# Kernel tuning notes

Hardware: AMD Instinct MI355X
Metric: run time of the kernel (lower is better)

The kernel has to match this reference:

```python
import jax, jax.numpy as jnp
import numpy as np

B, ISIZE, N, OSIZE = 2048, 512, 2048, 128
TC = 1.0 / 10.0  # dt/tau
PX = 0.5


def setup_inputs() -> dict:
    key = jax.random.key(0)
    ks = jax.random.split(key, 16)
    s = 0.01
    return {
        "x": jax.random.normal(ks[0], (B, ISIZE), jnp.float32),
        "h0_in": jax.random.normal(ks[1], (B, N), jnp.float32),
        "h1_in": jax.random.normal(ks[2], (B, N), jnp.float32),
        "h2_in": jax.random.normal(ks[3], (B, N), jnp.float32),
        "i_to_h0": s * jax.random.normal(ks[4], (ISIZE, N), jnp.float32),
        "h0_w": s * jax.random.normal(ks[5], (N, N), jnp.float32),
        "h0_b": s * jax.random.uniform(ks[6], (N,), jnp.float32),
        "h0_to_h1": s * jax.random.normal(ks[7], (N, N), jnp.float32),
        "h1_w": s * jax.random.normal(ks[8], (N, N), jnp.float32),
        "h1_b": s * jax.random.uniform(ks[9], (N,), jnp.float32),
        "h1_to_h2": s * jax.random.normal(ks[10], (N, N), jnp.float32),
        "h2_w": s * jax.random.normal(ks[11], (N, N), jnp.float32),
        "h2_b": s * jax.random.uniform(ks[12], (N,), jnp.float32),
        "w_out": s * jax.random.normal(ks[13], (N, OSIZE), jnp.float32),
        # Bernoulli(px) sparsity masks (non-trainable buffers in the original)
        "m01": (jax.random.uniform(ks[14], (N, N)) < PX).astype(jnp.float32),
        "m12": (jax.random.uniform(ks[15], (N, N)) < PX).astype(jnp.float32),
    }


def reference(x, h0_in, h1_in, h2_in, i_to_h0, h0_w, h0_b, h0_to_h1,
              h1_w, h1_b, h1_to_h2, h2_w, h2_b, w_out, m01, m12):
    tc = TC
    # zero-diagonal mask applied to every recurrent weight (no self-connections)
    diag = 1.0 - jnp.eye(N, dtype=h0_w.dtype)
    # replicate_ashok=True: feedforward weights are sparsified by Bernoulli masks
    h01 = h0_to_h1 * m01
    h12 = h1_to_h2 * m12

    # layer 0: input drive + masked recurrence + leaky integration
    h0 = h0_in * (1.0 - tc) + jax.nn.relu(
        x @ i_to_h0 + h0_in @ (h0_w * diag) + h0_b) * tc
    # layer 1
    h1 = h1_in * (1.0 - tc) + jax.nn.relu(
        h0 @ h01 + h1_in @ (h1_w * diag) + h1_b) * tc
    # layer 2
    h2 = h2_in * (1.0 - tc) + jax.nn.relu(
        h1 @ h12 + h2_in @ (h2_w * diag) + h2_b) * tc

    out = h2 @ w_out  # Linear without bias (replicate_ashok=True)
    return (h0, h1, h2, out)
```

## Files before the change

### kernel.cpp

```cpp
#include <hip/hip_runtime.h>
#include <hip/hip_bf16.h>
#include <stdint.h>

typedef __bf16 bf16;
typedef __bf16 bf16x8 __attribute__((ext_vector_type(8)));
typedef float f32x4 __attribute__((ext_vector_type(4)));

#define BB   2048
#define ISZ  512
#define NN   2048
#define OSZ  128

struct PackD { const float* src; bf16* dst; int W, ld, off, n8; };
struct TD    { const float* src; const float* msk; bf16* dst;
               int Ncols, ld_dst, k_off, mode, ntk, start; };
struct PAll  { PackD p[4]; TD d[7]; int packBlocks; };
struct TDef  { TD d[3]; int total; };

__global__ __launch_bounds__(256) void prep_all_k(PAll a) {
  if ((int)blockIdx.x < a.packBlocks) {
    int idx = blockIdx.x * 256 + threadIdx.x;
    PackD d = a.p[0]; int base = 0;
#pragma unroll
    for (int i = 1; i < 4; ++i) if (idx >= a.p[i - 1].n8) { d = a.p[i]; base = a.p[i - 1].n8; }
    if (idx >= d.n8) return;
    int e = (idx - base) * 8;
    int m = e / d.W;
    int c = e - m * d.W;
    const float4 v0 = *reinterpret_cast<const float4*>(d.src + e);
    const float4 v1 = *reinterpret_cast<const float4*>(d.src + e + 4);
    bf16x8 o;
    o[0] = (bf16)v0.x; o[1] = (bf16)v0.y; o[2] = (bf16)v0.z; o[3] = (bf16)v0.w;
    o[4] = (bf16)v1.x; o[5] = (bf16)v1.y; o[6] = (bf16)v1.z; o[7] = (bf16)v1.w;
    *reinterpret_cast<bf16x8*>(d.dst + (size_t)m * d.ld + d.off + c) = o;
    return;
  }
  int bid = blockIdx.x - a.packBlocks;
  TD d = a.d[0];
#pragma unroll
  for (int i = 1; i < 7; ++i) if (bid >= a.d[i].start) d = a.d[i];
  int local = bid - d.start;
  int k0 = (local % d.ntk) * 128;
  int n0 = (local / d.ntk) * 32;
  __shared__ float t[128][33];
  const int tx8 = threadIdx.x & 7;
  const int kr  = threadIdx.x >> 3;
  const int nc  = n0 + tx8 * 4;
#pragma unroll
  for (int i = 0; i < 4; ++i) {
    int k = k0 + kr + 32 * i;
    float4 v = *reinterpret_cast<const float4*>(d.src + (size_t)k * d.Ncols + nc);
    if (d.mode == 2) {
      float4 m = *reinterpret_cast<const float4*>(d.msk + (size_t)k * d.Ncols + nc);
      v.x *= m.x; v.y *= m.y; v.z *= m.z; v.w *= m.w;
    } else if (d.mode == 1) {
      if (k == nc)     v.x = 0.f;
      if (k == nc + 1) v.y = 0.f;
      if (k == nc + 2) v.z = 0.f;
      if (k == nc + 3) v.w = 0.f;
    }
    float* r = &t[kr + 32 * i][tx8 * 4];
    r[0] = v.x; r[1] = v.y; r[2] = v.z; r[3] = v.w;
  }
  __syncthreads();
  const int n  = threadIdx.x >> 3;
  const int kc = (threadIdx.x & 7) * 16;
  bf16x8 o0, o1;
#pragma unroll
  for (int j = 0; j < 8; ++j) {
    o0[j] = (bf16)t[kc + j][n];
    o1[j] = (bf16)t[kc + 8 + j][n];
  }
  bf16* dp = d.dst + (size_t)(n0 + n) * d.ld_dst + d.k_off + k0 + kc;
  *reinterpret_cast<bf16x8*>(dp) = o0;
  *reinterpret_cast<bf16x8*>(dp + 8) = o1;
}

struct GP {
  const bf16* A; const bf16* B;
  int K, lda, ldb;
  const float* hin; const float* bias; const float* radd;
  float* outf; int ld_out;
  bf16* nxt; int ld_nxt;
  int epi;
};

__device__ __forceinline__ void gload16(const bf16* g, bf16* l) {
  __builtin_amdgcn_global_load_lds(
      (const __attribute__((address_space(1))) void*)g,
      (__attribute__((address_space(3))) void*)l, 16, 0, 0);
}

__device__ __forceinline__ void epilogue_store(const GP& p, int row, int col, float v) {
  size_t oidx = (size_t)row * p.ld_out + col;
  if (p.epi == 0) {
    float pre = v + p.bias[col];
    if (p.radd) pre += p.radd[oidx];
    float h = p.hin[oidx] * 0.9f + fmaxf(pre, 0.f) * 0.1f;
    p.outf[oidx] = h;
    p.nxt[(size_t)row * p.ld_nxt + col] = (bf16)h;
  } else {
    p.outf[oidx] = v;
  }
}

__device__ __forceinline__ void gemm_ks(const GP p, uint8_t* smraw) {
  typedef bf16 smT[2][128][64];
  smT* sm = (smT*)smraw;
  const int lane = threadIdx.x & 63;
  const int wave = threadIdx.x >> 6;
  const int ks = wave >> 2;
  const int sp = wave & 3;
  const int gx = gridDim.x, nwg = gx * gridDim.y;
  const int lid = blockIdx.x + gx * blockIdx.y;
  const int q = nwg >> 3;
  const int swz = (lid & 7) * q + (lid >> 3);
  const int m0 = (swz / gx) * 128, n0 = (swz % gx) * 128;
  const int wm0 = (sp >> 1) * 64, wn0 = (sp & 1) * 64;
  const int srow = lane >> 3;
  const int scol = ((lane & 7) ^ srow) * 8;
  const int frow = lane & 15;
  const int rcol = (((ks << 2) + (lane >> 4)) ^ (frow & 7)) * 8;

  f32x4 acc[4][4];
#pragma unroll
  for (int i = 0; i < 4; ++i)
#pragma unroll
    for (int j = 0; j < 4; ++j)
#pragma unroll
      for (int r = 0; r < 4; ++r) acc[i][j][r] = 0.f;

  auto stage = [&](int buf, int t) {
    const int k0 = t * 64;
#pragma unroll
    for (int h = 0; h < 2; ++h) {
      const int c = wave + h * 8;
      gload16(p.A + (size_t)(m0 + c * 8 + srow) * p.lda + k0 + scol,
              &sm[buf][0][0][0] + c * 512);
      gload16(p.B + (size_t)(n0 + c * 8 + srow) * p.ldb + k0 + scol,
              &sm[buf][1][0][0] + c * 512);
    }
  };

  const int nt = p.K / 64;
  stage(0, 0);
  int cur = 0;
  for (int t = 0; t < nt; ++t) {
    if (t + 1 < nt) {
      stage(cur ^ 1, t + 1);
      asm volatile("s_waitcnt vmcnt(4)" ::: "memory");
    } else {
      asm volatile("s_waitcnt vmcnt(0)" ::: "memory");
    }
    __builtin_amdgcn_s_barrier();

    bf16x8 af[4], bf_[4];
#pragma unroll
    for (int i = 0; i < 4; ++i)
      af[i] = *reinterpret_cast<const bf16x8*>(&sm[cur][0][wm0 + i * 16 + frow][rcol]);
#pragma unroll
    for (int j = 0; j < 4; ++j)
      bf_[j] = *reinterpret_cast<const bf16x8*>(&sm[cur][1][wn0 + j * 16 + frow][rcol]);
#pragma unroll
    for (int i = 0; i < 4; ++i)
#pragma unroll
      for (int j = 0; j < 4; ++j)
        acc[i][j] = __builtin_amdgcn_mfma_f32_16x16x32_bf16(af[i], bf_[j], acc[i][j], 0, 0, 0);

    if (t + 1 < nt) {
      asm volatile("s_waitcnt lgkmcnt(0)" ::: "memory");
      __builtin_amdgcn_s_barrier();
    }
    cur ^= 1;
  }

  asm volatile("s_waitcnt lgkmcnt(0)" ::: "memory");
  __builtin_amdgcn_s_barrier();
  float* red = (float*)smraw;
  if (ks == 1) {
#pragma unroll
    for (int i = 0; i < 4; ++i)
#pragma unroll
      for (int j = 0; j < 4; ++j)
        *reinterpret_cast<f32x4*>(&red[sp * 4096 + (i * 4 + j) * 256 + lane * 4]) = acc[i][j];
    asm volatile("s_waitcnt lgkmcnt(0)" ::: "memory");
  }
  __builtin_amdgcn_s_barrier();
  if (ks == 0) {
#pragma unroll
    for (int i = 0; i < 4; ++i)
#pragma unroll
      for (int j = 0; j < 4; ++j) {
        f32x4 o = *reinterpret_cast<const f32x4*>(&red[sp * 4096 + (i * 4 + j) * 256 + lane * 4]);
#pragma unroll
        for (int r = 0; r < 4; ++r) acc[i][j][r] += o[r];
#pragma unroll
        for (int r = 0; r < 4; ++r)
          epilogue_store(p, m0 + wm0 + i * 16 + (lane >> 4) * 4 + r,
                         n0 + wn0 + j * 16 + (lane & 15), acc[i][j][r]);
      }
  }
}

__device__ __forceinline__ void transpose512(const TD& d, int tile, bool active,
                                             uint8_t* smraw) {
  float (*t)[65] = (float (*)[65])smraw;
  int k0 = 0, n0 = 0;
  if (active) { k0 = (tile % d.ntk) * 128; n0 = (tile / d.ntk) * 64; }
  const int tx = threadIdx.x & 15;
  const int kr = threadIdx.x >> 4;
  const int nc = n0 + tx * 4;
  if (active) {
#pragma unroll
    for (int i = 0; i < 4; ++i) {
      int k = k0 + kr + 32 * i;
      float4 v = *reinterpret_cast<const float4*>(d.src + (size_t)k * d.Ncols + nc);
      if (d.mode == 2) {
        float4 m = *reinterpret_cast<const float4*>(d.msk + (size_t)k * d.Ncols + nc);
        v.x *= m.x; v.y *= m.y; v.z *= m.z; v.w *= m.w;
      }
      float* r = &t[kr + 32 * i][tx * 4];
      r[0] = v.x; r[1] = v.y; r[2] = v.z; r[3] = v.w;
    }
  }
  __syncthreads();
  if (active) {
    const int n  = threadIdx.x >> 3;
    const int kc = (threadIdx.x & 7) * 16;
    bf16x8 o0, o1;
#pragma unroll
    for (int j = 0; j < 8; ++j) {
      o0[j] = (bf16)t[kc + j][n0 + n - n0 + n * 0 + n];
      o1[j] = (bf16)t[kc + 8 + j][n];
    }
#pragma unroll
    for (int j = 0; j < 8; ++j) o0[j] = (bf16)t[kc + j][n];
    bf16* dp = d.dst + (size_t)(n0 + n) * d.ld_dst + d.k_off + k0 + kc;
    *reinterpret_cast<bf16x8*>(dp) = o0;
    *reinterpret_cast<bf16x8*>(dp + 8) = o1;
  }
  __syncthreads();
}

__global__ __launch_bounds__(512) void k_tri(GP p0, GP p1, GP p2, TDef td) {
  __shared__ __align__(16) uint8_t smraw[65536];
  if (blockIdx.z < 3) {
    GP p;
    if (blockIdx.z == 0) p = p0;
    else if (blockIdx.z == 1) p = p1;
    else p = p2;
    gemm_ks(p, smraw);
    return;
  }
  const int bid = blockIdx.x + gridDim.x * blockIdx.y;
  const int nb = gridDim.x * gridDim.y;
  const int iters = (td.total + nb - 1) / nb;
  for (int it = 0; it < iters; ++it) {
    int tile = it * nb + bid;
    TD d = td.d[0];
    if (tile >= td.d[1].start) d = td.d[1];
    if (tile >= td.d[2].start) d = td.d[2];
    int local = tile - d.start;
    transpose512(d, local, tile < td.total, smraw);
  }
}

__global__ __launch_bounds__(512) void k_split(GP p0, GP p1) {
  __shared__ __align__(16) uint8_t smraw[65536];
  gemm_ks(blockIdx.z == 0 ? p0 : p1, smraw);
}

template<int BM, int BN>
__device__ __forceinline__ void gemm_body8(const GP p) {
  constexpr int BK = 32;
  constexpr int WM = BM / 2, WN = BN / 4;
  constexpr int FM = WM / 16, FN = WN / 16;
  __shared__ bf16 As[2][BM][BK];
  __shared__ bf16 Bs[2][BN][BK];
  const int lane = threadIdx.x & 63;
  const int wave = threadIdx.x >> 6;
  const int m0 = blockIdx.y * BM, n0 = blockIdx.x * BN;
  const int wm0 = (wave >> 2) * WM, wn0 = (wave & 3) * WN;
  const int srow = lane >> 2;
  const int scolE = (((lane & 3) ^ ((lane >> 3) & 3)) * 8);
  const int frow = lane & 15;
  const int rcolE = (((lane >> 4) ^ ((frow >> 1) & 3)) * 8);

  f32x4 acc[FM][FN];
#pragma unroll
  for (int i = 0; i < FM; ++i)
#pragma unroll
    for (int j = 0; j < FN; ++j)
#pragma unroll
      for (int r = 0; r < 4; ++r) acc[i][j][r] = 0.f;

  auto stage = [&](int buf, int t) {
    const int k0 = t * BK;
#pragma unroll
    for (int c = wave; c < BM / 16; c += 8) {
      const bf16* g = p.A + (size_t)(m0 + c * 16 + srow) * p.lda + k0 + scolE;
      gload16(g, &As[buf][0][0] + c * 512);
    }
#pragma unroll
    for (int c = wave; c < BN / 16; c += 8) {
      const bf16* g = p.B + (size_t)(n0 + c * 16 + srow) * p.ldb + k0 + scolE;
      gload16(g, &Bs[buf][0][0] + c * 512);
    }
  };

  const int nt = p.K / BK;
  stage(0, 0);
  __syncthreads();
  int cur = 0;
  for (int t = 0; t < nt; ++t) {
    if (t + 1 < nt) stage(cur ^ 1, t + 1);
    bf16x8 af[FM], bfrag[FN];
#pragma unroll
    for (int i = 0; i < FM; ++i)
      af[i] = *reinterpret_cast<const bf16x8*>(&As[cur][wm0 + i * 16 + frow][rcolE]);
#pragma unroll
    for (int j = 0; j < FN; ++j)
      bfrag[j] = *reinterpret_cast<const bf16x8*>(&Bs[cur][wn0 + j * 16 + frow][rcolE]);
#pragma unroll
    for (int i = 0; i < FM; ++i)
#pragma unroll
      for (int j = 0; j < FN; ++j)
        acc[i][j] = __builtin_amdgcn_mfma_f32_16x16x32_bf16(af[i], bfrag[j], acc[i][j], 0, 0, 0);
    __syncthreads();
    cur ^= 1;
  }

#pragma unroll
  for (int i = 0; i < FM; ++i)
#pragma unroll
    for (int j = 0; j < FN; ++j)
#pragma unroll
      for (int r = 0; r < 4; ++r)
        epilogue_store(p, m0 + wm0 + i * 16 + (lane >> 4) * 4 + r,
                       n0 + wn0 + j * 16 + (lane & 15), acc[i][j][r]);
}

__global__ __launch_bounds__(512) void k_out(GP p) { gemm_body8<32, 64>(p); }

__global__ __launch_bounds__(256) void k_epi(const float* __restrict__ P0,
                                             const float* __restrict__ P1,
                                             const float* __restrict__ radd,
                                             const float* __restrict__ hin,
                                             const float* __restrict__ bias,
                                             float* __restrict__ outf,
                                             bf16* __restrict__ nxt) {
  int e = (blockIdx.x * 256 + threadIdx.x) * 8;
  int colb = e & (NN - 1);
  const float4 a0 = *reinterpret_cast<const float4*>(P0 + e);
  const float4 a1 = *reinterpret_cast<const float4*>(P0 + e + 4);
  const float4 b0 = *reinterpret_cast<const float4*>(P1 + e);
  const float4 b1 = *reinterpret_cast<const float4*>(P1 + e + 4);
  const float4 r0 = *reinterpret_cast<const float4*>(radd + e);
  const float4 r1 = *reinterpret_cast<const float4*>(radd + e + 4);
  const float4 h0 = *reinterpret_cast<const float4*>(hin + e);
  const float4 h1 = *reinterpret_cast<const float4*>(hin + e + 4);
  const float4 c0 = *reinterpret_cast<const float4*>(bias + colb);
  const float4 c1 = *reinterpret_cast<const float4*>(bias + colb + 4);
  float pa[8] = {a0.x, a0.y, a0.z, a0.w, a1.x, a1.y, a1.z, a1.w};
  float pb[8] = {b0.x, b0.y, b0.z, b0.w, b1.x, b1.y, b1.z, b1.w};
  float pr[8] = {r0.x, r0.y, r0.z, r0.w, r1.x, r1.y, r1.z, r1.w};
  float ph[8] = {h0.x, h0.y, h0.z, h0.w, h1.x, h1.y, h1.z, h1.w};
  float pc[8] = {c0.x, c0.y, c0.z, c0.w, c1.x, c1.y, c1.z, c1.w};
  float4 o0, o1;
  bf16x8 nb;
#pragma unroll
  for (int j = 0; j < 8; ++j) {
    float pre = pa[j] + pb[j] + pr[j] + pc[j];
    float h = ph[j] * 0.9f + fmaxf(pre, 0.f) * 0.1f;
    (j < 4 ? (&o0.x)[j] : (&o1.x)[j - 4]) = h;
    nb[j] = (bf16)h;
  }
  *reinterpret_cast<float4*>(outf + e) = o0;
  *reinterpret_cast<float4*>(outf + e + 4) = o1;
  *reinterpret_cast<bf16x8*>(nxt + e) = nb;
}

extern "C" void kernel_launch(void* const* d_in, const int* in_sizes, int n_in,
                              void* d_out, int out_size, void* d_ws, size_t ws_size,
                              hipStream_t stream) {
  const float* x        = (const float*)d_in[0];
  const float* h0_in    = (const float*)d_in[1];
  const float* h1_in    = (const float*)d_in[2];
  const float* h2_in    = (const float*)d_in[3];
  const float* i_to_h0  = (const float*)d_in[4];
  const float* h0_w     = (const float*)d_in[5];
  const float* h0_b     = (const float*)d_in[6];
  const float* h0_to_h1 = (const float*)d_in[7];
  const float* h1_w     = (const float*)d_in[8];
  const float* h1_b     = (const float*)d_in[9];
  const float* h1_to_h2 = (const float*)d_in[10];
  const float* h2_w     = (const float*)d_in[11];
  const float* h2_b     = (const float*)d_in[12];
  const float* w_out    = (const float*)d_in[13];
  const float* m01      = (const float*)d_in[14];
  const float* m12      = (const float*)d_in[15];
  float* out = (float*)d_out;

  uint8_t* ws = (uint8_t*)d_ws;
  constexpr size_t OFF_A0  = 0;
  constexpr size_t OFF_W0  = OFF_A0 + 10485760;
  constexpr size_t OFF_W1R = OFF_W0 + 10485760;
  constexpr size_t OFF_W2R = OFF_W1R + 8388608;
  constexpr size_t OFF_W01 = OFF_W2R + 8388608;
  constexpr size_t OFF_W12 = OFF_W01 + 8388608;
  constexpr size_t OFF_WO  = OFF_W12 + 8388608;
  constexpr size_t OFF_AR1 = OFF_WO + 524288;
  constexpr size_t OFF_AR2 = OFF_AR1 + 8388608;
  constexpr size_t OFF_AH0 = OFF_AR2 + 8388608;
  constexpr size_t WS_NEED = OFF_AH0 + 8388608;
  if (ws_size < WS_NEED) return;

  bf16* A0  = (bf16*)(ws + OFF_A0);
  bf16* Wt0 = (bf16*)(ws + OFF_W0);
  bf16* W1r = (bf16*)(ws + OFF_W1R);
  bf16* W2r = (bf16*)(ws + OFF_W2R);
  bf16* W01 = (bf16*)(ws + OFF_W01);
  bf16* W12 = (bf16*)(ws + OFF_W12);
  bf16* WtO = (bf16*)(ws + OFF_WO);
  bf16* Ar1 = (bf16*)(ws + OFF_AR1);
  bf16* Ar2 = (bf16*)(ws + OFF_AR2);
  bf16* Ah0 = (bf16*)(ws + OFF_AH0);
  bf16* Ah1 = Ar1;
  bf16* Ah2 = Ar2;
  float* P0 = (float*)(ws + 0);
  float* P1 = (float*)(ws + 16777216);

  float* o_h0  = out;
  float* o_h1  = out + (size_t)BB * NN;
  float* o_h2  = out + (size_t)2 * BB * NN;
  float* o_out = out + (size_t)3 * BB * NN;

  PAll pa;
  int n8a = BB * ISZ / 8;
  int n8b = n8a + BB * NN / 8;
  int n8c = n8b + BB * NN / 8;
  int n8d = n8c + BB * NN / 8;
  pa.p[0] = {x,     A0,  ISZ, ISZ + NN, 0,   n8a};
  pa.p[1] = {h0_in, A0,  NN,  ISZ + NN, ISZ, n8b};
  pa.p[2] = {h1_in, Ar1, NN,  NN,       0,   n8c};
  pa.p[3] = {h2_in, Ar2, NN,  NN,       0,   n8d};
  pa.packBlocks = (n8d + 255) / 256;
  int s0 = 0;
  pa.d[0] = {i_to_h0, nullptr, Wt0, NN, ISZ + NN, 0,   0, ISZ / 128, s0}; s0 += (ISZ / 128) * (NN / 32);
  pa.d[1] = {h0_w,    nullptr, Wt0, NN, ISZ + NN, ISZ, 1, NN / 128,  s0}; s0 += (NN / 128) * (NN / 32);
  pa.d[2] = {h1_w,    nullptr, W1r, NN, NN,       0,   1, NN / 128,  s0}; s0 += (NN / 128) * (NN / 32);
  pa.d[3] = {h2_w,    nullptr, W2r, NN, NN,       0,   1, NN / 128,  s0}; s0 += (NN / 128) * (NN / 32);
  pa.d[4] = pa.d[3]; pa.d[4].start = 0x7FFFFFFF;
  pa.d[5] = pa.d[4];
  pa.d[6] = pa.d[4];
  prep_all_k<<<pa.packBlocks + s0, 256, 0, stream>>>(pa);

  TDef td;
  int t0 = 0;
  td.d[0] = {h0_to_h1, m01, W01, NN,  NN, 0, 2, NN / 128, t0}; t0 += (NN / 128) * (NN / 64);
  td.d[1] = {h1_to_h2, m12, W12, NN,  NN, 0, 2, NN / 128, t0}; t0 += (NN / 128) * (NN / 64);
  td.d[2] = {w_out,  nullptr, WtO, OSZ, NN, 0, 0, NN / 128, t0}; t0 += (NN / 128) * (OSZ / 64);
  td.total = t0;

  GP pS0{A0,  Wt0, ISZ + NN, ISZ + NN, ISZ + NN, h0_in, h0_b, nullptr,
         o_h0, NN, Ah0, NN, 0};
  GP pR1{Ar1, W1r, NN, NN, NN, nullptr, nullptr, nullptr, o_h1, NN, nullptr, 0, 1};
  GP pR2{Ar2, W2r, NN, NN, NN, nullptr, nullptr, nullptr, o_h2, NN, nullptr, 0, 1};
  k_tri<<<dim3(NN / 128, BB / 128, 4), 512, 0, stream>>>(pS0, pR1, pR2, td);

  GP pG1a{Ah0,          W01,          NN / 2, NN, NN, nullptr, nullptr, nullptr, P0, NN, nullptr, 0, 1};
  GP pG1b{Ah0 + NN / 2, W01 + NN / 2, NN / 2, NN, NN, nullptr, nullptr, nullptr, P1, NN, nullptr, 0, 1};
  k_split<<<dim3(NN / 128, BB / 128, 2), 512, 0, stream>>>(pG1a, pG1b);
  k_epi<<<BB * NN / 2048, 256, 0, stream>>>(P0, P1, o_h1, h1_in, h1_b, o_h1, Ah1);

  GP pG2a{Ah1,          W12,          NN / 2, NN, NN, nullptr, nullptr, nullptr, P0, NN, nullptr, 0, 1};
  GP pG2b{Ah1 + NN / 2, W12 + NN / 2, NN / 2, NN, NN, nullptr, nullptr, nullptr, P1, NN, nullptr, 0, 1};
  k_split<<<dim3(NN / 128, BB / 128, 2), 512, 0, stream>>>(pG2a, pG2b);
  k_epi<<<BB * NN / 2048, 256, 0, stream>>>(P0, P1, o_h2, h2_in, h2_b, o_h2, Ah2);

  GP pO{Ah2, WtO, NN, NN, NN, nullptr, nullptr, nullptr, o_out, OSZ, nullptr, 0, 1};
  k_out<<<dim3(OSZ / 64, BB / 32), 512, 0, stream>>>(pO);
}
```

Baseline: 214.4 us.

## Fuse feedforward GEMMs with leaky-ReLU epilogue, dropping split-K partials

Replaces the two-way split-K GEMM plus separate elementwise epilogue kernel for layers 1 and 2 with a single fused GEMM. It uses 128x64 tiles, an in-block K split across wave groups with an LDS reduction, and a grouped block-index swizzle, and it applies bias, the recurrent add, ReLU and the leaky update directly in the epilogue. This removes the fp32 partial buffers P0/P1, their round trips through global memory, and two kernel launches. In exchange each block now iterates over the full K of 2048, and the grid has the same block count but smaller tiles. A redundant store loop in the transpose is also cleaned up.

New measurement: 243.3 us. 1.14x slower.

```diff
diff --git a/kernel.cpp b/kernel.cpp
--- a/kernel.cpp
+++ b/kernel.cpp
@@ -202,6 +202,102 @@
   }
 }
 
+__device__ __forceinline__ void gemm_fused64(const GP p) {
+  __shared__ __align__(16) bf16 sA[2][128][64];
+  __shared__ __align__(16) bf16 sB[2][64][64];
+  const int lane = threadIdx.x & 63;
+  const int wave = threadIdx.x >> 6;
+  const int ks = wave >> 2;
+  const int sp = wave & 3;
+  const int gx = gridDim.x, nwg = gx * gridDim.y;
+  const int lid = blockIdx.x + gx * blockIdx.y;
+  const int q = nwg >> 3;
+  const int swz = (lid & 7) * q + (lid >> 3);
+  const int m0 = (swz / gx) * 128, n0 = (swz % gx) * 64;
+  const int wm0 = (sp >> 1) * 64, wn0 = (sp & 1) * 32;
+  const int srow = lane >> 3;
+  const int scol = ((lane & 7) ^ srow) * 8;
+  const int frow = lane & 15;
+  const int rcol = (((ks << 2) + (lane >> 4)) ^ (frow & 7)) * 8;
+
+  f32x4 acc[4][2];
+#pragma unroll
+  for (int i = 0; i < 4; ++i)
+#pragma unroll
+    for (int j = 0; j < 2; ++j)
+#pragma unroll
+      for (int r = 0; r < 4; ++r) acc[i][j][r] = 0.f;
+
+  auto stage = [&](int buf, int t) {
+    const int k0 = t * 64;
+    gload16(p.A + (size_t)(m0 + wave * 8 + srow) * p.lda + k0 + scol,
+            &sA[buf][0][0] + wave * 512);
+    gload16(p.A + (size_t)(m0 + (wave + 8) * 8 + srow) * p.lda + k0 + scol,
+            &sA[buf][0][0] + (wave + 8) * 512);
+    gload16(p.B + (size_t)(n0 + wave * 8 + srow) * p.ldb + k0 + scol,
+            &sB[buf][0][0] + wave * 512);
+  };
+
+  const int nt = p.K / 64;
+  stage(0, 0);
+  int cur = 0;
+  for (int t = 0; t < nt; ++t) {
+    if (t + 1 < nt) {
+      stage(cur ^ 1, t + 1);
+      asm volatile("s_waitcnt vmcnt(3)" ::: "memory");
+    } else {
+      asm volatile("s_waitcnt vmcnt(0)" ::: "memory");
+    }
+    __builtin_amdgcn_s_barrier();
+
+    bf16x8 af[4], bf_[2];
+#pragma unroll
+    for (int i = 0; i < 4; ++i)
+      af[i] = *reinterpret_cast<const bf16x8*>(&sA[cur][wm0 + i * 16 + frow][rcol]);
+#pragma unroll
+    for (int j = 0; j < 2; ++j)
+      bf_[j] = *reinterpret_cast<const bf16x8*>(&sB[cur][wn0 + j * 16 + frow][rcol]);
+#pragma unroll
+    for (int i = 0; i < 4; ++i)
+#pragma unroll
+      for (int j = 0; j < 2; ++j)
+        acc[i][j] = __builtin_amdgcn_mfma_f32_16x16x32_bf16(af[i], bf_[j], acc[i][j], 0, 0, 0);
+
+    if (t + 1 < nt) {
+      asm volatile("s_waitcnt lgkmcnt(0)" ::: "memory");
+      __builtin_amdgcn_s_barrier();
+    }
+    cur ^= 1;
+  }
+
+  asm volatile("s_waitcnt lgkmcnt(0)" ::: "memory");
+  __builtin_amdgcn_s_barrier();
+  float* red = (float*)&sA[0][0][0];
+  if (ks == 1) {
+#pragma unroll
+    for (int i = 0; i < 4; ++i)
+#pragma unroll
+      for (int j = 0; j < 2; ++j)
+        *reinterpret_cast<f32x4*>(&red[sp * 2048 + (i * 2 + j) * 256 + lane * 4]) = acc[i][j];
+    asm volatile("s_waitcnt lgkmcnt(0)" ::: "memory");
+  }
+  __builtin_amdgcn_s_barrier();
+  if (ks == 0) {
+#pragma unroll
+    for (int i = 0; i < 4; ++i)
+#pragma unroll
+      for (int j = 0; j < 2; ++j) {
+        f32x4 o = *reinterpret_cast<const f32x4*>(&red[sp * 2048 + (i * 2 + j) * 256 + lane * 4]);
+#pragma unroll
+        for (int r = 0; r < 4; ++r) acc[i][j][r] += o[r];
+#pragma unroll
+        for (int r = 0; r < 4; ++r)
+          epilogue_store(p, m0 + wm0 + i * 16 + (lane >> 4) * 4 + r,
+                         n0 + wn0 + j * 16 + (lane & 15), acc[i][j][r]);
+      }
+  }
+}
+
 __device__ __forceinline__ void transpose512(const TD& d, int tile, bool active,
                                              uint8_t* smraw) {
   float (*t)[65] = (float (*)[65])smraw;
@@ -230,11 +326,9 @@
     bf16x8 o0, o1;
 #pragma unroll
     for (int j = 0; j < 8; ++j) {
-      o0[j] = (bf16)t[kc + j][n0 + n - n0 + n * 0 + n];
+      o0[j] = (bf16)t[kc + j][n];
       o1[j] = (bf16)t[kc + 8 + j][n];
     }
-#pragma unroll
-    for (int j = 0; j < 8; ++j) o0[j] = (bf16)t[kc + j][n];
     bf16* dp = d.dst + (size_t)(n0 + n) * d.ld_dst + d.k_off + k0 + kc;
     *reinterpret_cast<bf16x8*>(dp) = o0;
     *reinterpret_cast<bf16x8*>(dp + 8) = o1;
@@ -265,10 +359,7 @@
   }
 }
 
-__global__ __launch_bounds__(512) void k_split(GP p0, GP p1) {
-  __shared__ __align__(16) uint8_t smraw[65536];
-  gemm_ks(blockIdx.z == 0 ? p0 : p1, smraw);
-}
+__global__ __launch_bounds__(512) void k_fused(GP p) { gemm_fused64(p); }
 
 template<int BM, int BN>
 __device__ __forceinline__ void gemm_body8(const GP p) {
@@ -341,44 +432,6 @@
 }
 
 __global__ __launch_bounds__(512) void k_out(GP p) { gemm_body8<32, 64>(p); }
-
-__global__ __launch_bounds__(256) void k_epi(const float* __restrict__ P0,
-                                             const float* __restrict__ P1,
-                                             const float* __restrict__ radd,
-                                             const float* __restrict__ hin,
-                                             const float* __restrict__ bias,
-                                             float* __restrict__ outf,
-                                             bf16* __restrict__ nxt) {
-  int e = (blockIdx.x * 256 + threadIdx.x) * 8;
-  int colb = e & (NN - 1);
-  const float4 a0 = *reinterpret_cast<const float4*>(P0 + e);
-  const float4 a1 = *reinterpret_cast<const float4*>(P0 + e + 4);
-  const float4 b0 = *reinterpret_cast<const float4*>(P1 + e);
-  const float4 b1 = *reinterpret_cast<const float4*>(P1 + e + 4);
-  const float4 r0 = *reinterpret_cast<const float4*>(radd + e);
-  const float4 r1 = *reinterpret_cast<const float4*>(radd + e + 4);
-  const float4 h0 = *reinterpret_cast<const float4*>(hin + e);
-  const float4 h1 = *reinterpret_cast<const float4*>(hin + e + 4);
-  const float4 c0 = *reinterpret_cast<const float4*>(bias + colb);
-  const float4 c1 = *reinterpret_cast<const float4*>(bias + colb + 4);
-  float pa[8] = {a0.x, a0.y, a0.z, a0.w, a1.x, a1.y, a1.z, a1.w};
-  float pb[8] = {b0.x, b0.y, b0.z, b0.w, b1.x, b1.y, b1.z, b1.w};
-  float pr[8] = {r0.x, r0.y, r0.z, r0.w, r1.x, r1.y, r1.z, r1.w};
-  float ph[8] = {h0.x, h0.y, h0.z, h0.w, h1.x, h1.y, h1.z, h1.w};
-  float pc[8] = {c0.x, c0.y, c0.z, c0.w, c1.x, c1.y, c1.z, c1.w};
-  float4 o0, o1;
-  bf16x8 nb;
-#pragma unroll
-  for (int j = 0; j < 8; ++j) {
-    float pre = pa[j] + pb[j] + pr[j] + pc[j];
-    float h = ph[j] * 0.9f + fmaxf(pre, 0.f) * 0.1f;
-    (j < 4 ? (&o0.x)[j] : (&o1.x)[j - 4]) = h;
-    nb[j] = (bf16)h;
-  }
-  *reinterpret_cast<float4*>(outf + e) = o0;
-  *reinterpret_cast<float4*>(outf + e + 4) = o1;
-  *reinterpret_cast<bf16x8*>(nxt + e) = nb;
-}
 
 extern "C" void kernel_launch(void* const* d_in, const int* in_sizes, int n_in,
                               void* d_out, int out_size, void* d_ws, size_t ws_size,
@@ -427,8 +480,6 @@
   bf16* Ah0 = (bf16*)(ws + OFF_AH0);
   bf16* Ah1 = Ar1;
   bf16* Ah2 = Ar2;
-  float* P0 = (float*)(ws + 0);
-  float* P1 = (float*)(ws + 16777216);
 
   float* o_h0  = out;
   float* o_h1  = out + (size_t)BB * NN;
@@ -468,15 +519,11 @@
   GP pR2{Ar2, W2r, NN, NN, NN, nullptr, nullptr, nullptr, o_h2, NN, nullptr, 0, 1};
   k_tri<<<dim3(NN / 128, BB / 128, 4), 512, 0, stream>>>(pS0, pR1, pR2, td);
 
-  GP pG1a{Ah0,          W01,          NN / 2, NN, NN, nullptr, nullptr, nullptr, P0, NN, nullptr, 0, 1};
-  GP pG1b{Ah0 + NN / 2, W01 + NN / 2, NN / 2, NN, NN, nullptr, nullptr, nullptr, P1, NN, nullptr, 0, 1};
-  k_split<<<dim3(NN / 128, BB / 128, 2), 512, 0, stream>>>(pG1a, pG1b);
-  k_epi<<<BB * NN / 2048, 256, 0, stream>>>(P0, P1, o_h1, h1_in, h1_b, o_h1, Ah1);
-
-  GP pG2a{Ah1,          W12,          NN / 2, NN, NN, nullptr, nullptr, nullptr, P0, NN, nullptr, 0, 1};
-  GP pG2b{Ah1 + NN / 2, W12 + NN / 2, NN / 2, NN, NN, nullptr, nullptr, nullptr, P1, NN, nullptr, 0, 1};
-  k_split<<<dim3(NN / 128, BB / 128, 2), 512, 0, stream>>>(pG2a, pG2b);
-  k_epi<<<BB * NN / 2048, 256, 0, stream>>>(P0, P1, o_h2, h2_in, h2_b, o_h2, Ah2);
+  GP pF1{Ah0, W01, NN, NN, NN, h1_in, h1_b, o_h1, o_h1, NN, Ah1, NN, 0};
+  k_fused<<<dim3(NN / 64, BB / 128), 512, 0, stream>>>(pF1);
+
+  GP pF2{Ah1, W12, NN, NN, NN, h2_in, h2_b, o_h2, o_h2, NN, Ah2, NN, 0};
+  k_fused<<<dim3(NN / 64, BB / 128), 512, 0, stream>>>(pF2);
 
   GP pO{Ah2, WtO, NN, NN, NN, nullptr, nullptr, nullptr, o_out, OSZ, nullptr, 0, 1};
   k_out<<<dim3(OSZ / 64, BB / 32), 512, 0, stream>>>(pO);
```
